# Kernel optimization log

Hardware: AMD Instinct MI355X
Metric: run time of the kernel (lower is better)

Reference implementation:

```python
import jax, jax.numpy as jnp
import numpy as np
from jax import lax

# --- COSMO-SAC constants (defaults from the layer) ---
T = 623.15
Q0 = 79.53
R0 = 66.69
C_HB = 85580.0
RGAS = 8.3144598 / 4184.0
SIG_HB = 0.0084
EPS = 3.667
AEFF = 7.5
EO = 0.0002395
ZC = 10.0
X0 = 0.235
X1 = 1.0 - 0.235
N_SIGMA = 51
N_ITERS = 50


def _deltaw():
    s = np.linspace(-0.025, 0.025, N_SIGMA)
    sigma_m = np.tile(s, (N_SIGMA, 1))          # rows of grid values
    sigma_n = sigma_m.T
    sigma_acc = np.tril(sigma_n) + np.triu(sigma_m, 1)
    sigma_don = np.tril(sigma_m) + np.triu(sigma_n, 1)
    fpol = (EPS - 1.0) / (EPS + 0.5)
    alpha = 0.3 * AEFF ** 1.5 / EO
    alpha_prime = fpol * alpha
    dw = (alpha_prime / 2.0 * (sigma_m + sigma_n) ** 2
          + C_HB * np.maximum(0.0, sigma_acc - SIG_HB) * np.minimum(0.0, sigma_don + SIG_HB))
    return jnp.asarray(dw, jnp.float32)

DELTAW = _deltaw()                       # [51,51]
SSS = jnp.exp(-DELTAW / (RGAS * T))      # [51,51]


def get_Gamma(psigma):
    """50-step fixed-point solve. psigma: [B,51] -> Gamma: [B,51]."""
    AA = SSS[None, :, :] * psigma[:, None, :]   # [B,51,51]
    def step(G, _):
        Gnew = 1.0 / jnp.einsum('bmn,bn->bm', AA, G)
        return (Gnew + G) * 0.5, None
    G, _ = lax.scan(step, jnp.ones_like(psigma), None, length=N_ITERS)
    return G


def setup_inputs() -> dict:
    key = jax.random.key(0)
    k1, k2, k3, k4 = jax.random.split(key, 4)
    B = 32768
    return {
        "input_my_sigma": jax.random.uniform(k1, (B, N_SIGMA), dtype=jnp.float32),
        "v_compound": jax.random.uniform(k2, (B,), dtype=jnp.float32),
        "input_vt_sigma": jax.random.uniform(k3, (B, N_SIGMA, 2), dtype=jnp.float32),
        "v_vt": jax.random.uniform(k4, (B,), dtype=jnp.float32),
    }


def reference(input_my_sigma, v_compound, input_vt_sigma, v_vt):
    my = input_my_sigma                 # [B,51]
    vt = input_vt_sigma[:, :, 1]        # [B,51]
    A0 = jnp.sum(my, axis=1)            # [B]
    A1 = jnp.sum(vt, axis=1)            # [B]

    psigma_mix = (X0 * my + X1 * vt) / (X0 * A0[:, None] + X1 * A1[:, None])
    lnGamma_mix = jnp.log(get_Gamma(psigma_mix))       # [B,51]

    # residual part for component i = 0
    psigma = my / A0[:, None]
    lnGammai = jnp.log(get_Gamma(psigma))              # [B,51]
    lng_resid = A0 / AEFF * jnp.sum(psigma * (lnGamma_mix - lnGammai), axis=1)

    # combinatorial part (Staverman-Guggenheim)
    q0 = A0 / Q0
    q1 = A1 / Q0
    r0 = v_compound / R0
    r1 = v_vt / R0
    xq = X0 * q0 + X1 * q1
    xr = X0 * r0 + X1 * r1
    theta = X0 * q0 / xq
    phi = X0 * r0 / xr
    l0 = ZC / 2.0 * (r0 - q0) - (r0 - 1.0)
    l1 = ZC / 2.0 * (r1 - q1) - (r1 - 1.0)
    xl = X0 * l0 + X1 * l1
    lng_comb = (jnp.log(phi / X0) + ZC / 2.0 * q0 * jnp.log(theta / phi)
                + l0 - phi / X0 * xl)

    return (lng_resid + lng_comb)[:, None]             # [B,1]
```

## Files before the change

### kernel.cpp

```cpp
#include <hip/hip_runtime.h>

typedef __bf16 bf16;
typedef __attribute__((ext_vector_type(4))) bf16 bf16x4;
typedef __attribute__((ext_vector_type(8))) bf16 bf16x8;
typedef __attribute__((ext_vector_type(4))) float f32x4;

namespace {

constexpr int NITERS = 50;

constexpr double csqrt(double x) {
  double s = x > 1 ? x : 1;
  for (int i = 0; i < 60; ++i) s = 0.5 * (s + x / s);
  return s;
}
constexpr double AP_D =
    ((3.667 - 1.0) / (3.667 + 0.5)) * (0.3 * (7.5 * csqrt(7.5)) / 0.0002395);
constexpr double RGAST_D = (8.3144598 / 4184.0) * 623.15;

__device__ __forceinline__ float sss_val(int i, int j) {
  if (i > 50 || j > 50) return 0.0f;
  const float si = -0.025f + 0.001f * (float)i;
  const float sj = -0.025f + 0.001f * (float)j;
  const float acc = fmaxf(0.0f, fmaxf(si, sj) - 0.0084f);
  const float don = fminf(0.0f, fminf(si, sj) + 0.0084f);
  const float dw = (float)(AP_D * 0.5) * (si + sj) * (si + sj) + 85580.0f * acc * don;
  return expf(-dw * (float)(1.0 / RGAST_D));
}

__device__ __forceinline__ int slot2row(int slot) {
  if (slot < 48) return slot;
  if ((slot & 3) == 0 && slot < 60) return 48 + ((slot - 48) >> 2);
  return 99;
}

__device__ __forceinline__ float fast_log(float x) {
  return __builtin_amdgcn_logf(x) * 0.69314718056f;
}

__device__ __forceinline__ f32x4 mfma(bf16x8 a, bf16x8 b, f32x4 c) {
  return __builtin_amdgcn_mfma_f32_16x16x32_bf16(a, b, c, 0, 0, 0);
}

}

__global__ __launch_bounds__(256, 4) void cosmo_mfma_trim(
    const float* __restrict__ my_sigma,
    const float* __restrict__ v_comp,
    const float* __restrict__ vt_sigma,
    const float* __restrict__ v_vt,
    float* __restrict__ out,
    int B)
{
  const int lane = threadIdx.x & 63;
  const int wv   = threadIdx.x >> 6;
  const int s    = lane & 15;
  const int g    = lane >> 4;
  const int e    = blockIdx.x * 32 + wv * 8 + (s >> 1);
  const int task = s & 1;
  const bool ein = (e < B);
  const int  ec  = ein ? e : 0;

  float A0, A1, wC[13];
  {
    float myv[13], vtv[13];
#pragma unroll
    for (int t = 0; t < 4; ++t)
#pragma unroll
      for (int r = 0; r < 4; ++r) {
        const int li = 4 * t + r;
        if (li >= 13) continue;
        const int n  = slot2row(16 * t + 4 * g + r);
        const bool nv = (n < 51) && ein;
        const int nc = (n < 51) ? n : 50;
        myv[li] = nv ? my_sigma[(size_t)ec * 51 + nc] : 0.0f;
        vtv[li] = nv ? vt_sigma[((size_t)ec * 51 + nc) * 2 + 1] : 0.0f;
      }
    float pA0 = 0.f, pA1 = 0.f;
#pragma unroll
    for (int i = 0; i < 13; ++i) { pA0 += myv[i]; pA1 += vtv[i]; }
    A0 = pA0; A0 += __shfl_xor(A0, 16, 64); A0 += __shfl_xor(A0, 32, 64);
    A1 = pA1; A1 += __shfl_xor(A1, 16, 64); A1 += __shfl_xor(A1, 32, 64);

    const float den  = task ? (0.235f * A0 + 0.765f * A1) : A0;
    const float rden = __builtin_amdgcn_rcpf(den);
#pragma unroll
    for (int i = 0; i < 13; ++i) {
      const float num = task ? (0.235f * myv[i] + 0.765f * vtv[i]) : myv[i];
      wC[i] = num * rden;
    }
  }

  float Gt[13];
#pragma unroll
  for (int i = 0; i < 13; ++i) Gt[i] = wC[i];

  bf16x8 afr[4][2];
#pragma unroll
  for (int tp = 0; tp < 4; ++tp)
#pragma unroll
    for (int kt = 0; kt < 2; ++kt) {
      bf16x8 v;
#pragma unroll
      for (int i = 0; i < 8; ++i) {
        const int kslot = 16 * (2 * kt + (i >> 2)) + 4 * g + (i & 3);
        v[i] = (bf16)sss_val(slot2row(16 * tp + s), slot2row(kslot));
      }
      afr[tp][kt] = v;
    }

  f32x4 pad3;
  pad3[0] = (g == 3) ? 1.0f : 0.0f;
  pad3[1] = pad3[2] = pad3[3] = 1.0f;

  const bf16 bz = (bf16)0.0f;

#pragma unroll 1
  for (int it = 0; it < NITERS; ++it) {
    bf16x4 hb[4];
#pragma unroll
    for (int t = 0; t < 3; ++t)
#pragma unroll
      for (int r = 0; r < 4; ++r)
        hb[t][r] = (bf16)Gt[4 * t + r];
    hb[3][0] = (bf16)Gt[12];
    hb[3][1] = bz; hb[3][2] = bz; hb[3][3] = bz;

    const bf16x8 b0 = __builtin_shufflevector(hb[0], hb[1], 0, 1, 2, 3, 4, 5, 6, 7);
    const bf16x8 b1 = __builtin_shufflevector(hb[2], hb[3], 0, 1, 2, 3, 4, 5, 6, 7);

    const f32x4 z = {};
    f32x4 acc[4];
#pragma unroll
    for (int tp = 0; tp < 3; ++tp) acc[tp] = mfma(afr[tp][0], b0, z);
    acc[3] = mfma(afr[3][0], b0, pad3);
#pragma unroll
    for (int tp = 0; tp < 4; ++tp) acc[tp] = mfma(afr[tp][1], b1, acc[tp]);

#pragma unroll
    for (int tp = 0; tp < 3; ++tp)
#pragma unroll
      for (int r = 0; r < 4; ++r) {
        const int i = 4 * tp + r;
        const float rc = __builtin_amdgcn_rcpf(acc[tp][r]);
        Gt[i] = 0.5f * __builtin_fmaf(wC[i], rc, Gt[i]);
      }
    {
      const float rc = __builtin_amdgcn_rcpf(acc[3][0]);
      Gt[12] = 0.5f * __builtin_fmaf(wC[12], rc, Gt[12]);
    }
  }

  const float rA0 = __builtin_amdgcn_rcpf(A0);
  float Sp = 0.f;
#pragma unroll
  for (int t = 0; t < 4; ++t)
#pragma unroll
    for (int r = 0; r < 4; ++r) {
      const int li = 4 * t + r;
      if (li >= 13) continue;
      const int n = slot2row(16 * t + 4 * g + r);
      if (n < 51) {
        const float p  = (ein ? my_sigma[(size_t)ec * 51 + n] : 0.0f) * rA0;
        const float gg = (wC[li] != 0.0f)
                           ? Gt[li] * __builtin_amdgcn_rcpf(wC[li]) : 1.0f;
        Sp += p * __builtin_amdgcn_logf(gg);
      }
    }
  Sp += __shfl_xor(Sp, 16, 64);
  Sp += __shfl_xor(Sp, 32, 64);
  const float St = Sp * 0.69314718056f;
  const float So = __shfl_xor(St, 1, 64);

  if (task == 0 && g == 0 && ein) {
    const float lng_resid = A0 * (1.0f / 7.5f) * (So - St);
    const float v0  = v_comp[e];
    const float v1v = v_vt[e];
    const float q0 = A0 * (1.0f / 79.53f), q1 = A1 * (1.0f / 79.53f);
    const float r0 = v0 * (1.0f / 66.69f), r1 = v1v * (1.0f / 66.69f);
    const float xq = 0.235f * q0 + 0.765f * q1;
    const float xr = 0.235f * r0 + 0.765f * r1;
    const float theta = 0.235f * q0 * __builtin_amdgcn_rcpf(xq);
    const float phi   = 0.235f * r0 * __builtin_amdgcn_rcpf(xr);
    const float l0 = 5.0f * (r0 - q0) - (r0 - 1.0f);
    const float l1 = 5.0f * (r1 - q1) - (r1 - 1.0f);
    const float xl = 0.235f * l0 + 0.765f * l1;
    const float lng_comb = fast_log(phi * (1.0f / 0.235f))
                         + 5.0f * q0 * fast_log(theta * __builtin_amdgcn_rcpf(phi))
                         + l0 - (phi * (1.0f / 0.235f)) * xl;
    out[e] = lng_resid + lng_comb;
  }
}

extern "C" void kernel_launch(void* const* d_in, const int* in_sizes, int n_in,
                              void* d_out, int out_size, void* d_ws, size_t ws_size,
                              hipStream_t stream) {
  const float* my  = (const float*)d_in[0];
  const float* vc  = (const float*)d_in[1];
  const float* vts = (const float*)d_in[2];
  const float* vvt = (const float*)d_in[3];
  float* out = (float*)d_out;
  const int B = in_sizes[1];
  const int grid = (B + 31) / 32;
  cosmo_mfma_trim<<<grid, 256, 0, stream>>>(my, vc, vts, vvt, out, B);
}
```

Before: 111.7 us.

## Replace late-iteration reciprocals with Newton refinement and pack bf16 via cvt_pk

The fixed-point loop now runs its first 16 iterations with the hardware reciprocal. The remaining iterations refine the previous reciprocal with one Newton step (fma plus mul) instead of calling v_rcp. The 0.5 damping is folded into a pre-halved weight, and bf16 packing uses the packed v_cvt_pk_bf16_f32 instruction. MFMA issue is wrapped in s_setprio. The aim is to shorten the per-iteration dependency chain and cut transcendental and conversion instruction count. This relies on the accumulator changing slowly between iterations, which puts accuracy at risk if convergence is poor.

```diff
diff --git a/kernel.cpp b/kernel.cpp
--- a/kernel.cpp
+++ b/kernel.cpp
@@ -1,13 +1,13 @@
 #include <hip/hip_runtime.h>
 
 typedef __bf16 bf16;
-typedef __attribute__((ext_vector_type(4))) bf16 bf16x4;
 typedef __attribute__((ext_vector_type(8))) bf16 bf16x8;
 typedef __attribute__((ext_vector_type(4))) float f32x4;
 
 namespace {
 
 constexpr int NITERS = 50;
+constexpr int KEXACT = 16;
 
 constexpr double csqrt(double x) {
   double s = x > 1 ? x : 1;
@@ -42,9 +42,17 @@
   return __builtin_amdgcn_mfma_f32_16x16x32_bf16(a, b, c, 0, 0, 0);
 }
 
-}
-
-__global__ __launch_bounds__(256, 4) void cosmo_mfma_trim(
+__device__ __forceinline__ unsigned cvt_pk(float lo, float hi) {
+  unsigned r;
+  asm("v_cvt_pk_bf16_f32 %0, %1, %2" : "=v"(r) : "v"(lo), "v"(hi));
+  return r;
+}
+
+union B8 { unsigned u[4]; bf16x8 v; };
+
+}
+
+__global__ __launch_bounds__(256, 4) void cosmo_mfma_r6(
     const float* __restrict__ my_sigma,
     const float* __restrict__ v_comp,
     const float* __restrict__ vt_sigma,
@@ -56,12 +64,13 @@
   const int wv   = threadIdx.x >> 6;
   const int s    = lane & 15;
   const int g    = lane >> 4;
+  const int task = s & 1;
   const int e    = blockIdx.x * 32 + wv * 8 + (s >> 1);
-  const int task = s & 1;
   const bool ein = (e < B);
   const int  ec  = ein ? e : 0;
 
-  float A0, A1, wC[13];
+  float A0, A1;
+  float wh[13], Gt[13], rc[13];
   {
     float myv[13], vtv[13];
 #pragma unroll
@@ -79,21 +88,21 @@
     float pA0 = 0.f, pA1 = 0.f;
 #pragma unroll
     for (int i = 0; i < 13; ++i) { pA0 += myv[i]; pA1 += vtv[i]; }
-    A0 = pA0; A0 += __shfl_xor(A0, 16, 64); A0 += __shfl_xor(A0, 32, 64);
-    A1 = pA1; A1 += __shfl_xor(A1, 16, 64); A1 += __shfl_xor(A1, 32, 64);
-
-    const float den  = task ? (0.235f * A0 + 0.765f * A1) : A0;
+    pA0 += __shfl_xor(pA0, 16, 64); pA0 += __shfl_xor(pA0, 32, 64);
+    pA1 += __shfl_xor(pA1, 16, 64); pA1 += __shfl_xor(pA1, 32, 64);
+    A0 = pA0; A1 = pA1;
+
+    const float den  = task ? (0.235f * pA0 + 0.765f * pA1) : pA0;
     const float rden = __builtin_amdgcn_rcpf(den);
+    const float rdh  = 0.5f * rden;
 #pragma unroll
     for (int i = 0; i < 13; ++i) {
       const float num = task ? (0.235f * myv[i] + 0.765f * vtv[i]) : myv[i];
-      wC[i] = num * rden;
+      Gt[i] = num * rden;
+      wh[i] = num * rdh;
+      rc[i] = 1.0f;
     }
   }
-
-  float Gt[13];
-#pragma unroll
-  for (int i = 0; i < 13; ++i) Gt[i] = wC[i];
 
   bf16x8 afr[4][2];
 #pragma unroll
@@ -113,43 +122,72 @@
   pad3[0] = (g == 3) ? 1.0f : 0.0f;
   pad3[1] = pad3[2] = pad3[3] = 1.0f;
 
-  const bf16 bz = (bf16)0.0f;
-
-#pragma unroll 1
-  for (int it = 0; it < NITERS; ++it) {
-    bf16x4 hb[4];
-#pragma unroll
-    for (int t = 0; t < 3; ++t)
-#pragma unroll
-      for (int r = 0; r < 4; ++r)
-        hb[t][r] = (bf16)Gt[4 * t + r];
-    hb[3][0] = (bf16)Gt[12];
-    hb[3][1] = bz; hb[3][2] = bz; hb[3][3] = bz;
-
-    const bf16x8 b0 = __builtin_shufflevector(hb[0], hb[1], 0, 1, 2, 3, 4, 5, 6, 7);
-    const bf16x8 b1 = __builtin_shufflevector(hb[2], hb[3], 0, 1, 2, 3, 4, 5, 6, 7);
+  f32x4 acc[4];
+
+  auto matvec = [&]() {
+    B8 x0, x1;
+    x0.u[0] = cvt_pk(Gt[0],  Gt[1]);
+    x0.u[1] = cvt_pk(Gt[2],  Gt[3]);
+    x0.u[2] = cvt_pk(Gt[4],  Gt[5]);
+    x0.u[3] = cvt_pk(Gt[6],  Gt[7]);
+    x1.u[0] = cvt_pk(Gt[8],  Gt[9]);
+    x1.u[1] = cvt_pk(Gt[10], Gt[11]);
+    x1.u[2] = cvt_pk(Gt[12], 0.0f);
+    x1.u[3] = 0;
+    const bf16x8 b0 = x0.v, b1 = x1.v;
 
     const f32x4 z = {};
-    f32x4 acc[4];
+    __builtin_amdgcn_s_setprio(1);
 #pragma unroll
     for (int tp = 0; tp < 3; ++tp) acc[tp] = mfma(afr[tp][0], b0, z);
     acc[3] = mfma(afr[3][0], b0, pad3);
 #pragma unroll
     for (int tp = 0; tp < 4; ++tp) acc[tp] = mfma(afr[tp][1], b1, acc[tp]);
-
+    __builtin_amdgcn_s_setprio(0);
+  };
+
+  auto upd_rcp = [&]() {
 #pragma unroll
     for (int tp = 0; tp < 3; ++tp)
 #pragma unroll
       for (int r = 0; r < 4; ++r) {
         const int i = 4 * tp + r;
-        const float rc = __builtin_amdgcn_rcpf(acc[tp][r]);
-        Gt[i] = 0.5f * __builtin_fmaf(wC[i], rc, Gt[i]);
+        const float rcv = __builtin_amdgcn_rcpf(acc[tp][r]);
+        rc[i] = rcv;
+        Gt[i] = __builtin_fmaf(wh[i], rcv, 0.5f * Gt[i]);
       }
     {
-      const float rc = __builtin_amdgcn_rcpf(acc[3][0]);
-      Gt[12] = 0.5f * __builtin_fmaf(wC[12], rc, Gt[12]);
-    }
-  }
+      const float rcv = __builtin_amdgcn_rcpf(acc[3][0]);
+      rc[12] = rcv;
+      Gt[12] = __builtin_fmaf(wh[12], rcv, 0.5f * Gt[12]);
+    }
+  };
+
+  auto upd_newton = [&]() {
+#pragma unroll
+    for (int tp = 0; tp < 3; ++tp)
+#pragma unroll
+      for (int r = 0; r < 4; ++r) {
+        const int i = 4 * tp + r;
+        const float nr  = __builtin_fmaf(-acc[tp][r], rc[i], 2.0f);
+        const float rcv = rc[i] * nr;
+        rc[i] = rcv;
+        Gt[i] = __builtin_fmaf(wh[i], rcv, 0.5f * Gt[i]);
+      }
+    {
+      const float nr  = __builtin_fmaf(-acc[3][0], rc[12], 2.0f);
+      const float rcv = rc[12] * nr;
+      rc[12] = rcv;
+      Gt[12] = __builtin_fmaf(wh[12], rcv, 0.5f * Gt[12]);
+    }
+  };
+
+  matvec();
+#pragma unroll 1
+  for (int it = 0; it < KEXACT; ++it) { upd_rcp(); matvec(); }
+#pragma unroll 1
+  for (int it = KEXACT; it < NITERS - 1; ++it) { upd_newton(); matvec(); }
+  upd_newton();
 
   const float rA0 = __builtin_amdgcn_rcpf(A0);
   float Sp = 0.f;
@@ -162,8 +200,8 @@
       const int n = slot2row(16 * t + 4 * g + r);
       if (n < 51) {
         const float p  = (ein ? my_sigma[(size_t)ec * 51 + n] : 0.0f) * rA0;
-        const float gg = (wC[li] != 0.0f)
-                           ? Gt[li] * __builtin_amdgcn_rcpf(wC[li]) : 1.0f;
+        const float gg = (wh[li] != 0.0f)
+                           ? Gt[li] * (0.5f * __builtin_amdgcn_rcpf(wh[li])) : 1.0f;
         Sp += p * __builtin_amdgcn_logf(gg);
       }
     }
@@ -202,5 +240,5 @@
   float* out = (float*)d_out;
   const int B = in_sizes[1];
   const int grid = (B + 31) / 32;
-  cosmo_mfma_trim<<<grid, 256, 0, stream>>>(my, vc, vts, vvt, out, B);
-}
+  cosmo_mfma_r6<<<grid, 256, 0, stream>>>(my, vc, vts, vvt, out, B);
+}
```

Measured after the change: 109.5 us. No clear change (-1.9%).
